# Optimization experiments

Hardware: AMD Instinct MI355X
Metric: run time of the kernel (lower is better)

The kernel has to match this reference:

```python
import jax, jax.numpy as jnp
import numpy as np

EPS = 1e-7  # K.epsilon()
ROUTINGS = 3


def squash(v, axis=-1):
    s2 = jnp.sum(jnp.square(v), axis=axis, keepdims=True)
    scale = s2 / (1.0 + s2) / jnp.sqrt(s2 + EPS)
    return scale * v


def setup_inputs() -> dict:
    key = jax.random.key(0)
    k1, k2 = jax.random.split(key)
    B, J, I = 32, 2048, 16   # batch, input_num_capsule, input_dim_capsule
    N, D = 64, 32            # num_capsule, dim_capsule
    x = jax.random.normal(k1, (B, J, I), dtype=jnp.float32)
    W = jax.random.normal(k2, (N, J, D, I), dtype=jnp.float32) * 0.05
    return {"x": x, "W": W}


def reference(x, W):
    # inputs_hat[b,n,j,d] = sum_i W[n,j,d,i] * x[b,j,i]
    u_hat = jnp.einsum('bji,njdi->bnjd', x, W)
    B, N, J, D = u_hat.shape
    b = jnp.zeros((B, N, J), dtype=u_hat.dtype)
    v = None
    for r in range(ROUTINGS):
        c = jax.nn.softmax(b, axis=1)                 # softmax over num_capsule
        s = jnp.einsum('bnj,bnjd->bnd', c, u_hat)     # weighted sum over input caps
        v = squash(s)                                  # [B, N, D]
        if r < ROUTINGS - 1:
            b = b + jnp.einsum('bnd,bnjd->bnj', v, u_hat)
    return v
```

## Files before the change

### kernel.cpp

```cpp
#include <hip/hip_runtime.h>
#include <math.h>

#define JJ 2048
#define II 16
#define NN 64
#define DD 32
#define BBATCH 32

#define JC 16
#define THREADS 512
#define BSUB 16

typedef unsigned int u32;

__device__ __forceinline__ void gload_lds16(const void* g, void* l) {
    __builtin_amdgcn_global_load_lds(
        (const __attribute__((address_space(1))) u32*)g,
        (__attribute__((address_space(3))) u32*)l, 16, 0, 0);
}

template <int MODE>
__global__ __launch_bounds__(THREADS, 2)
void caps_pass(const float* __restrict__ xg, const float* __restrict__ Wg,
               const float* __restrict__ vsumg, float* __restrict__ s)
{
    __shared__ float qb0[NN * DD * 4];
    __shared__ float qb1[NN * DD * 4];
    __shared__ float qb2[NN * DD * 4];
    __shared__ float qb3[NN * DD * 4];
    __shared__ float xs[BSUB * JC * II];
    __shared__ float lpb[2][BSUB][NN];

    const int t    = threadIdx.x;
    const int lane = t & 63;
    const int w    = t >> 6;
    const int bq   = w >> 1;
    const int dh   = w & 1;
    const int n    = lane;

    const int id = blockIdx.x;
    const int jc = (id & 7) + ((id >> 4) << 3);
    const int bh = (id >> 3) & 1;
    const int j0 = jc * JC;
    const int b0 = bh * BSUB;

    float vs[4][16];
    if (MODE) {
        #pragma unroll
        for (int bb = 0; bb < 4; ++bb) {
            const float* vp = vsumg + ((size_t)(b0 + bq * 4 + bb) * NN + n) * DD + dh * 16;
            #pragma unroll
            for (int dq = 0; dq < 4; ++dq) {
                const float4 v4 = *(const float4*)(vp + dq * 4);
                vs[bb][dq * 4 + 0] = v4.x; vs[bb][dq * 4 + 1] = v4.y;
                vs[bb][dq * 4 + 2] = v4.z; vs[bb][dq * 4 + 3] = v4.w;
            }
        }
    }
    asm volatile("s_waitcnt vmcnt(0)" ::: "memory");
    if (MODE) {
        #pragma unroll
        for (int bb = 0; bb < 4; ++bb)
            #pragma unroll
            for (int dd = 0; dd < 16; ++dd)
                asm volatile("" :: "v"(vs[bb][dd]));
    }

    #pragma unroll
    for (int it = 0; it < 2; ++it) {
        const int T = t + it * THREADS;
        const int p = T >> 2, quad = T & 3;
        const int bl = p >> 4, jj = p & 15;
        const float* src = xg + ((size_t)(b0 + bl) * JJ + (j0 + jj)) * II + quad * 4;
        gload_lds16(src, xs + (size_t)T * 4);
    }

    auto issueQ = [&](int Qi, float* buf) {
        const int Q  = Qi > 63 ? 63 : Qi;
        const int jq = Q >> 2, q = Q & 3;
        #pragma unroll
        for (int it = 0; it < 4; ++it) {
            const int T    = t + it * THREADS;
            const int nrow = T >> 5;
            const int dsl  = T & 31;
            const int d    = dsl ^ (nrow & 7);
            const float* src = Wg + ((size_t)nrow * JJ + (j0 + jq)) * (DD * II) + d * II + q * 4;
            gload_lds16(src, buf + (size_t)T * 4);
        }
    };

    float uh[4][16];
    float sacc[4][16];
    #pragma unroll
    for (int bb = 0; bb < 4; ++bb)
        #pragma unroll
        for (int dd = 0; dd < 16; ++dd) { uh[bb][dd] = 0.f; sacc[bb][dd] = 0.f; }

    auto computeQ = [&](int jj, int q, const float* buf) {
        float4 xq[4];
        #pragma unroll
        for (int bb = 0; bb < 4; ++bb)
            xq[bb] = ((const float4*)xs)[((bq * 4 + bb) * JC + jj) * 4 + q];
        const float4* bv = (const float4*)buf;
        #pragma unroll
        for (int dg = 0; dg < 4; ++dg) {
            float4 wv[4];
            #pragma unroll
            for (int u = 0; u < 4; ++u) {
                const int dd = dg * 4 + u;
                const int slot = (dh * 16 + dd) ^ (n & 7);
                wv[u] = bv[n * 32 + slot];
            }
            #pragma unroll
            for (int u = 0; u < 4; ++u) {
                const int dd = dg * 4 + u;
                #pragma unroll
                for (int bb = 0; bb < 4; ++bb) {
                    uh[bb][dd] = fmaf(wv[u].x, xq[bb].x, uh[bb][dd]);
                    uh[bb][dd] = fmaf(wv[u].y, xq[bb].y, uh[bb][dd]);
                    uh[bb][dd] = fmaf(wv[u].z, xq[bb].z, uh[bb][dd]);
                    uh[bb][dd] = fmaf(wv[u].w, xq[bb].w, uh[bb][dd]);
                }
            }
        }
    };

    auto finishJ = [&]() {
        if (MODE) {
            float lp[4];
            #pragma unroll
            for (int bb = 0; bb < 4; ++bb) {
                float acc = 0.f;
                #pragma unroll
                for (int dd = 0; dd < 16; ++dd) acc = fmaf(uh[bb][dd], vs[bb][dd], acc);
                lp[bb] = acc;
                lpb[dh][bq * 4 + bb][n] = acc;
            }
            asm volatile("s_waitcnt lgkmcnt(0)" ::: "memory");
            __builtin_amdgcn_s_barrier();
            asm volatile("" ::: "memory");
            #pragma unroll
            for (int bb = 0; bb < 4; ++bb) lp[bb] += lpb[1 - dh][bq * 4 + bb][n];
            #pragma unroll
            for (int bb = 0; bb < 4; ++bb) {
                float m = lp[bb];
                #pragma unroll
                for (int off = 1; off < 64; off <<= 1) m = fmaxf(m, __shfl_xor(m, off));
                const float e = __expf(lp[bb] - m);
                float es = e;
                #pragma unroll
                for (int off = 1; off < 64; off <<= 1) es += __shfl_xor(es, off);
                const float c = e / es;
                #pragma unroll
                for (int dd = 0; dd < 16; ++dd) {
                    sacc[bb][dd] = fmaf(c, uh[bb][dd], sacc[bb][dd]);
                    uh[bb][dd] = 0.f;
                }
            }
        } else {
            #pragma unroll
            for (int bb = 0; bb < 4; ++bb)
                #pragma unroll
                for (int dd = 0; dd < 16; ++dd) {
                    sacc[bb][dd] += uh[bb][dd];
                    uh[bb][dd] = 0.f;
                }
        }
    };

    float* bufs[4] = { qb0, qb1, qb2, qb3 };
    issueQ(0, bufs[0]);
    issueQ(1, bufs[1]);

    for (int jj = 0; jj < JC; ++jj) {
        #pragma unroll
        for (int q = 0; q < 4; ++q) {
            const int k = jj * 4 + q;
            asm volatile("s_waitcnt vmcnt(4)" ::: "memory");
            __builtin_amdgcn_s_barrier();
            asm volatile("" ::: "memory");
            issueQ(k + 2, bufs[(q + 2) & 3]);
            computeQ(jj, q, bufs[q]);
        }
        finishJ();
    }

    const float cs = MODE ? 1.0f : (1.0f / 64.0f);
    #pragma unroll
    for (int bb = 0; bb < 4; ++bb) {
        float* sp = s + ((size_t)(b0 + bq * 4 + bb) * NN + n) * DD + dh * 16;
        #pragma unroll
        for (int dd = 0; dd < 16; ++dd)
            atomicAdd(sp + dd, sacc[bb][dd] * cs);
    }
}

__global__ __launch_bounds__(256)
void caps_squash(const float* __restrict__ s, float* __restrict__ vsum,
                 float* __restrict__ out) {
    const int idx = blockIdx.x * 256 + threadIdx.x;
    const float sv = s[idx];
    float sq = sv * sv;
    sq += __shfl_xor(sq, 1);
    sq += __shfl_xor(sq, 2);
    sq += __shfl_xor(sq, 4);
    sq += __shfl_xor(sq, 8);
    sq += __shfl_xor(sq, 16);
    const float s2 = sq;
    const float scale = s2 / (1.0f + s2) / sqrtf(s2 + 1e-7f);
    const float v = scale * sv;
    out[idx] = v;
    vsum[idx] += v;
}

extern "C" void kernel_launch(void* const* d_in, const int* in_sizes, int n_in,
                              void* d_out, int out_size, void* d_ws, size_t ws_size,
                              hipStream_t stream) {
    const float* x = (const float*)d_in[0];
    const float* W = (const float*)d_in[1];
    float* out = (float*)d_out;

    float* s    = (float*)d_ws;
    float* vsum = s + BBATCH * NN * DD;

    const size_t sbytes = (size_t)BBATCH * NN * DD * sizeof(float);
    const int sqblocks = (BBATCH * NN * DD) / 256;

    hipMemsetAsync(s, 0, 2 * sbytes, stream);

    caps_pass<0><<<256, THREADS, 0, stream>>>(x, W, vsum, s);
    caps_squash<<<sqblocks, 256, 0, stream>>>(s, vsum, out);

    hipMemsetAsync(s, 0, sbytes, stream);
    caps_pass<1><<<256, THREADS, 0, stream>>>(x, W, vsum, s);
    caps_squash<<<sqblocks, 256, 0, stream>>>(s, vsum, out);

    hipMemsetAsync(s, 0, sbytes, stream);
    caps_pass<1><<<256, THREADS, 0, stream>>>(x, W, vsum, s);
    caps_squash<<<sqblocks, 256, 0, stream>>>(s, vsum, out);
}
```

Measured before the change: 3.286 ms.

## Restage W chunks by d-quarter, reload vsum per j, and accumulate directly in pass 0

Each LDS stage now holds a quarter of the d rows with all i values, instead of all d with a quarter of i. Each stage's work becomes complete dot4 products per output, using a full 32-way XOR swizzle. The 64 vsum registers are no longer kept live across the loop; they are reloaded from global memory at the end of each j, which cuts register pressure at the cost of extra loads and a vmcnt(0) stall. Pass 0 accumulates straight into sacc and drops the uh array and its per-j fold.

```diff
diff --git a/kernel.cpp b/kernel.cpp
--- a/kernel.cpp
+++ b/kernel.cpp
@@ -19,52 +19,33 @@
         (__attribute__((address_space(3))) u32*)l, 16, 0, 0);
 }
 
+__device__ __forceinline__ float dot4(const float4 a, const float4 b) {
+    return fmaf(a.x, b.x, fmaf(a.y, b.y, fmaf(a.z, b.z, a.w * b.w)));
+}
+
 template <int MODE>
 __global__ __launch_bounds__(THREADS, 2)
 void caps_pass(const float* __restrict__ xg, const float* __restrict__ Wg,
                const float* __restrict__ vsumg, float* __restrict__ s)
 {
-    __shared__ float qb0[NN * DD * 4];
-    __shared__ float qb1[NN * DD * 4];
-    __shared__ float qb2[NN * DD * 4];
-    __shared__ float qb3[NN * DD * 4];
+    __shared__ float qb0[NN * DD * II / 4];
+    __shared__ float qb1[NN * DD * II / 4];
+    __shared__ float qb2[NN * DD * II / 4];
+    __shared__ float qb3[NN * DD * II / 4];
     __shared__ float xs[BSUB * JC * II];
     __shared__ float lpb[2][BSUB][NN];
 
     const int t    = threadIdx.x;
-    const int lane = t & 63;
+    const int n    = t & 63;
     const int w    = t >> 6;
     const int bq   = w >> 1;
     const int dh   = w & 1;
-    const int n    = lane;
 
     const int id = blockIdx.x;
     const int jc = (id & 7) + ((id >> 4) << 3);
     const int bh = (id >> 3) & 1;
     const int j0 = jc * JC;
     const int b0 = bh * BSUB;
-
-    float vs[4][16];
-    if (MODE) {
-        #pragma unroll
-        for (int bb = 0; bb < 4; ++bb) {
-            const float* vp = vsumg + ((size_t)(b0 + bq * 4 + bb) * NN + n) * DD + dh * 16;
-            #pragma unroll
-            for (int dq = 0; dq < 4; ++dq) {
-                const float4 v4 = *(const float4*)(vp + dq * 4);
-                vs[bb][dq * 4 + 0] = v4.x; vs[bb][dq * 4 + 1] = v4.y;
-                vs[bb][dq * 4 + 2] = v4.z; vs[bb][dq * 4 + 3] = v4.w;
-            }
-        }
-    }
-    asm volatile("s_waitcnt vmcnt(0)" ::: "memory");
-    if (MODE) {
-        #pragma unroll
-        for (int bb = 0; bb < 4; ++bb)
-            #pragma unroll
-            for (int dd = 0; dd < 16; ++dd)
-                asm volatile("" :: "v"(vs[bb][dd]));
-    }
 
     #pragma unroll
     for (int it = 0; it < 2; ++it) {
@@ -75,16 +56,18 @@
         gload_lds16(src, xs + (size_t)T * 4);
     }
 
-    auto issueQ = [&](int Qi, float* buf) {
-        const int Q  = Qi > 63 ? 63 : Qi;
-        const int jq = Q >> 2, q = Q & 3;
+    auto issueG = [&](int Gi, float* buf) {
+        const int G  = Gi > 63 ? 63 : Gi;
+        const int jg = G >> 2, dq = G & 3;
         #pragma unroll
         for (int it = 0; it < 4; ++it) {
-            const int T    = t + it * THREADS;
-            const int nrow = T >> 5;
-            const int dsl  = T & 31;
-            const int d    = dsl ^ (nrow & 7);
-            const float* src = Wg + ((size_t)nrow * JJ + (j0 + jq)) * (DD * II) + d * II + q * 4;
+            const int T  = t + it * THREADS;
+            const int nr = T >> 5;
+            const int sl = T & 31;
+            const int l  = sl ^ (nr & 31);
+            const int dr = l >> 2, iq = l & 3;
+            const float* src = Wg + ((size_t)nr * JJ + (j0 + jg)) * (DD * II)
+                                  + (dq + dr * 4) * II + iq * 4;
             gload_lds16(src, buf + (size_t)T * 4);
         }
     };
@@ -94,55 +77,81 @@
     #pragma unroll
     for (int bb = 0; bb < 4; ++bb)
         #pragma unroll
-        for (int dd = 0; dd < 16; ++dd) { uh[bb][dd] = 0.f; sacc[bb][dd] = 0.f; }
-
-    auto computeQ = [&](int jj, int q, const float* buf) {
-        float4 xq[4];
-        #pragma unroll
-        for (int bb = 0; bb < 4; ++bb)
-            xq[bb] = ((const float4*)xs)[((bq * 4 + bb) * JC + jj) * 4 + q];
+        for (int dd = 0; dd < 16; ++dd) { sacc[bb][dd] = 0.f; if (MODE) uh[bb][dd] = 0.f; }
+
+    auto computeG = [&](int jj, int q, const float* buf) {
         const float4* bv = (const float4*)buf;
-        #pragma unroll
-        for (int dg = 0; dg < 4; ++dg) {
-            float4 wv[4];
-            #pragma unroll
-            for (int u = 0; u < 4; ++u) {
-                const int dd = dg * 4 + u;
-                const int slot = (dh * 16 + dd) ^ (n & 7);
-                wv[u] = bv[n * 32 + slot];
+        const float4* xv = (const float4*)xs;
+        #pragma unroll
+        for (int iq = 0; iq < 4; ++iq) {
+            float4 xqb[4];
+            #pragma unroll
+            for (int bb = 0; bb < 4; ++bb)
+                xqb[bb] = xv[((bq * 4 + bb) * JC + jj) * 4 + iq];
+            #pragma unroll
+            for (int drp = 0; drp < 4; ++drp) {
+                const int l  = (dh * 4 + drp) * 4 + iq;
+                const int sl = l ^ (n & 31);
+                const float4 w4 = bv[n * 32 + sl];
+                const int dd = q + drp * 4;
+                #pragma unroll
+                for (int bb = 0; bb < 4; ++bb) {
+                    float& acc = MODE ? uh[bb][dd] : sacc[bb][dd];
+                    acc += dot4(w4, xqb[bb]);
+                }
             }
-            #pragma unroll
-            for (int u = 0; u < 4; ++u) {
-                const int dd = dg * 4 + u;
-                #pragma unroll
-                for (int bb = 0; bb < 4; ++bb) {
-                    uh[bb][dd] = fmaf(wv[u].x, xq[bb].x, uh[bb][dd]);
-                    uh[bb][dd] = fmaf(wv[u].y, xq[bb].y, uh[bb][dd]);
-                    uh[bb][dd] = fmaf(wv[u].z, xq[bb].z, uh[bb][dd]);
-                    uh[bb][dd] = fmaf(wv[u].w, xq[bb].w, uh[bb][dd]);
-                }
-            }
         }
     };
 
-    auto finishJ = [&]() {
+    float* bufs[4] = { qb0, qb1, qb2, qb3 };
+    issueG(0, bufs[0]);
+    issueG(1, bufs[1]);
+
+    for (int jj = 0; jj < JC; ++jj) {
+        #pragma unroll
+        for (int q = 0; q < 4; ++q) {
+            asm volatile("s_waitcnt vmcnt(4)" ::: "memory");
+            __builtin_amdgcn_s_barrier();
+            asm volatile("" ::: "memory");
+            issueG(jj * 4 + q + 2, bufs[(q + 2) & 3]);
+            computeG(jj, q, bufs[q]);
+        }
         if (MODE) {
             float lp[4];
             #pragma unroll
-            for (int bb = 0; bb < 4; ++bb) {
-                float acc = 0.f;
-                #pragma unroll
-                for (int dd = 0; dd < 16; ++dd) acc = fmaf(uh[bb][dd], vs[bb][dd], acc);
-                lp[bb] = acc;
-                lpb[dh][bq * 4 + bb][n] = acc;
+            for (int bp = 0; bp < 2; ++bp) {
+                float4 vsl[2][4];
+                #pragma unroll
+                for (int u = 0; u < 2; ++u) {
+                    const int bb = bp * 2 + u;
+                    const float4* vp = (const float4*)(vsumg
+                        + ((size_t)(b0 + bq * 4 + bb) * NN + n) * DD + dh * 16);
+                    #pragma unroll
+                    for (int q4 = 0; q4 < 4; ++q4) vsl[u][q4] = vp[q4];
+                }
+                asm volatile("s_waitcnt vmcnt(0)" ::: "memory");
+                #pragma unroll
+                for (int u = 0; u < 2; ++u) {
+                    const int bb = bp * 2 + u;
+                    float acc = 0.f;
+                    #pragma unroll
+                    for (int q4 = 0; q4 < 4; ++q4) {
+                        acc = fmaf(uh[bb][q4 * 4 + 0], vsl[u][q4].x, acc);
+                        acc = fmaf(uh[bb][q4 * 4 + 1], vsl[u][q4].y, acc);
+                        acc = fmaf(uh[bb][q4 * 4 + 2], vsl[u][q4].z, acc);
+                        acc = fmaf(uh[bb][q4 * 4 + 3], vsl[u][q4].w, acc);
+                    }
+                    lp[bb] = acc;
+                }
             }
+            #pragma unroll
+            for (int bb = 0; bb < 4; ++bb) lpb[dh][bq * 4 + bb][n] = lp[bb];
             asm volatile("s_waitcnt lgkmcnt(0)" ::: "memory");
             __builtin_amdgcn_s_barrier();
             asm volatile("" ::: "memory");
             #pragma unroll
-            for (int bb = 0; bb < 4; ++bb) lp[bb] += lpb[1 - dh][bq * 4 + bb][n];
-            #pragma unroll
             for (int bb = 0; bb < 4; ++bb) {
+                lp[bb] += lpb[1 - dh][bq * 4 + bb][n];
                 float m = lp[bb];
                 #pragma unroll
                 for (int off = 1; off < 64; off <<= 1) m = fmaxf(m, __shfl_xor(m, off));
@@ -157,32 +166,7 @@
                     uh[bb][dd] = 0.f;
                 }
             }
-        } else {
-            #pragma unroll
-            for (int bb = 0; bb < 4; ++bb)
-                #pragma unroll
-                for (int dd = 0; dd < 16; ++dd) {
-                    sacc[bb][dd] += uh[bb][dd];
-                    uh[bb][dd] = 0.f;
-                }
-        }
-    };
-
-    float* bufs[4] = { qb0, qb1, qb2, qb3 };
-    issueQ(0, bufs[0]);
-    issueQ(1, bufs[1]);
-
-    for (int jj = 0; jj < JC; ++jj) {
-        #pragma unroll
-        for (int q = 0; q < 4; ++q) {
-            const int k = jj * 4 + q;
-            asm volatile("s_waitcnt vmcnt(4)" ::: "memory");
-            __builtin_amdgcn_s_barrier();
-            asm volatile("" ::: "memory");
-            issueQ(k + 2, bufs[(q + 2) & 3]);
-            computeQ(jj, q, bufs[q]);
-        }
-        finishJ();
+        }
     }
 
     const float cs = MODE ? 1.0f : (1.0f / 64.0f);
```

Result: slower. 4.192 ms (+27.6%).
